# Kernel optimization log

Hardware: AMD Instinct MI355X
Metric: run time of the kernel (lower is better)

The kernel has to match this reference:

```python
import jax, jax.numpy as jnp
import numpy as np

EPS = 1e-6


def _att_vector(x, W, b, sharp2, th2, is_last):
    """AttentionVector on a 2D payoff slice.
    x: (N, a, m). W: (1, 2), b: (1,). Returns (N, a)."""
    # compare_param: pair (x[n,j,k], x[n,i,k]) -> Linear(2,1) -> sigmoid -> mean over k
    # Linear on the concat pair is w00*x[n,j,k] + w01*x[n,i,k] + b, so we fuse it.
    lin = W[0, 0] * x[:, None, :, :] + W[0, 1] * x[:, :, None, :] + b[0]  # (N,a,a,m)
    c = jnp.mean(jax.nn.sigmoid(lin), axis=3)  # (N,a,a)
    # max_normalize over dim 2
    c = c / (jnp.max(c, axis=2, keepdims=True) + EPS)
    # compute_player_mask
    m = jnp.mean(c, axis=2)  # (N,a)
    m = jax.nn.relu(m * sharp2[0] + th2[0])
    m = jax.nn.softmax(m, axis=1)
    if not is_last:
        m = m / (jnp.max(m, axis=1, keepdims=True) + EPS)
    return m


def setup_inputs() -> dict:
    key = jax.random.key(0)
    ks = jax.random.split(key, 16)
    N, a1, a2, f = 128, 64, 64, 2
    inp = {
        "x": jax.random.normal(ks[0], (N, f, a1, a2), dtype=jnp.float32),
        "fc_W": jax.random.normal(ks[1], (2, 2), dtype=jnp.float32) * 0.5,
        "fc_b": jax.random.normal(ks[2], (2,), dtype=jnp.float32) * 0.1,
        "p1_W": jax.random.normal(ks[3], (1, 2), dtype=jnp.float32) * 0.5,
        "p1_b": jax.random.normal(ks[4], (1,), dtype=jnp.float32) * 0.1,
        "p1_sharp": jnp.ones((1,), dtype=jnp.float32),
        "p1_th": jnp.zeros((1,), dtype=jnp.float32),
        "p2_W": jax.random.normal(ks[5], (1, 2), dtype=jnp.float32) * 0.5,
        "p2_b": jax.random.normal(ks[6], (1,), dtype=jnp.float32) * 0.1,
        "p2_sharp": jnp.ones((1,), dtype=jnp.float32),
        "p2_th": jnp.zeros((1,), dtype=jnp.float32),
        "out_W": jax.random.normal(ks[7], (1, 2), dtype=jnp.float32) * 0.5,
        "out_b": jax.random.normal(ks[8], (1,), dtype=jnp.float32) * 0.1,
        "out_sharp": jnp.ones((1,), dtype=jnp.float32),
        "out_th": jnp.zeros((1,), dtype=jnp.float32),
    }
    return inp


def reference(x, fc_W, fc_b, p1_W, p1_b, p1_sharp, p1_th,
              p2_W, p2_b, p2_sharp, p2_th,
              out_W, out_b, out_sharp, out_th):
    # x: (N, f=2, a1, a2) -> (N, a1, a2, f)
    h = jnp.transpose(x, (0, 2, 3, 1))
    # is_fc_first: Linear(2, 2) + ReLU on last dim
    h = jax.nn.relu(h @ fc_W.T + fc_b)  # (N,a1,a2,2)
    # one AttentionModule (module_layers=1, not simult)
    vec1 = _att_vector(h[..., 0], p1_W, p1_b, p1_sharp, p1_th, is_last=False)  # (N,a1)
    h = h * vec1[:, :, None, None]
    pl2 = jnp.transpose(h[..., 1], (0, 2, 1))  # (N,a2,a1)
    vec2 = _att_vector(pl2, p2_W, p2_b, p2_sharp, p2_th, is_last=False)  # (N,a2)
    h = h * vec2[:, None, :, None]
    # with_last: final AttentionVector (is_last=True) on player-1 channel
    out = _att_vector(h[..., 0], out_W, out_b, out_sharp, out_th, is_last=True)  # (N,a1)
    return out
```

## Files before the change

### kernel.cpp

```cpp
#include <hip/hip_runtime.h>


constexpr int A   = 64;
constexpr int PAD = 68;
constexpr float L2E  = 1.4426950408889634f;
constexpr float EPSF = 1e-6f;

__device__ __forceinline__ float bcast(float v, int srcLane) {
    return __int_as_float(__builtin_amdgcn_readlane(__float_as_int(v), srcLane));
}
__device__ __forceinline__ float rcpf(float v) { return __builtin_amdgcn_rcpf(v); }
__device__ __forceinline__ float ex2(float v)  { return __builtin_amdgcn_exp2f(v); }

template <int CTRL>
__device__ __forceinline__ float upd_dpp(float src) {
    return __int_as_float(__builtin_amdgcn_update_dpp(
        0, __float_as_int(src), CTRL, 0xF, 0xF, true));
}
__device__ __forceinline__ float wave_sum64(float x) {
    x += upd_dpp<0x111>(x);
    x += upd_dpp<0x112>(x);
    x += upd_dpp<0x114>(x);
    x += upd_dpp<0x118>(x);
    x += upd_dpp<0x142>(x);
    x += upd_dpp<0x143>(x);
    return bcast(x, 63);
}
__device__ __forceinline__ float wave_max64(float x) {
    x = fmaxf(x, upd_dpp<0x111>(x));
    x = fmaxf(x, upd_dpp<0x112>(x));
    x = fmaxf(x, upd_dpp<0x114>(x));
    x = fmaxf(x, upd_dpp<0x118>(x));
    x = fmaxf(x, upd_dpp<0x142>(x));
    x = fmaxf(x, upd_dpp<0x143>(x));
    return bcast(x, 63);
}

__device__ __forceinline__ void att2q(const float* __restrict__ prow,
                                      const float* __restrict__ qL,
                                      int row0, int lane,
                                      float* __restrict__ mbuf,
                                      float* __restrict__ mg)
{
    const float qreg0 = qL[row0 * PAD + lane];
    const float qreg1 = qL[(row0 + 1) * PAD + lane];
    float acc0 = 0.f, acc1 = 0.f;
#pragma unroll 1
    for (int c = 0; c < 4; ++c) {
        float pk[16];
        *(float4*)(&pk[0])  = *(const float4*)(prow + c * 16 + 0);
        *(float4*)(&pk[4])  = *(const float4*)(prow + c * 16 + 4);
        *(float4*)(&pk[8])  = *(const float4*)(prow + c * 16 + 8);
        *(float4*)(&pk[12]) = *(const float4*)(prow + c * 16 + 12);
#pragma unroll
        for (int t = 0; t < 8; ++t) {
            const int k0 = c * 16 + 2 * t, k1 = k0 + 1;
            {
                float u0 = fmaf(pk[2 * t],     bcast(qreg0, k0), 1.0f);
                float u1 = fmaf(pk[2 * t + 1], bcast(qreg0, k1), 1.0f);
                acc0 = fmaf(u0 + u1, rcpf(u0 * u1), acc0);
            }
            {
                float u0 = fmaf(pk[2 * t],     bcast(qreg1, k0), 1.0f);
                float u1 = fmaf(pk[2 * t + 1], bcast(qreg1, k1), 1.0f);
                acc1 = fmaf(u0 + u1, rcpf(u0 * u1), acc1);
            }
        }
    }
    const float s0 = wave_sum64(acc0), m0 = wave_max64(acc0);
    const float s1 = wave_sum64(acc1), m1 = wave_max64(acc1);
    if (lane == 0) {
        float v0 = (s0 * (1.0f / 4096.0f)) / (m0 * (1.0f / 64.0f) + EPSF);
        float v1 = (s1 * (1.0f / 4096.0f)) / (m1 * (1.0f / 64.0f) + EPSF);
        mbuf[row0]     = v0;
        mbuf[row0 + 1] = v1;
        __hip_atomic_store(mg + row0,     v0 + 2.0f, __ATOMIC_RELAXED, __HIP_MEMORY_SCOPE_AGENT);
        __hip_atomic_store(mg + row0 + 1, v1 + 2.0f, __ATOMIC_RELAXED, __HIP_MEMORY_SCOPE_AGENT);
    }
}

__device__ __forceinline__ float softmax64(float m, float sharp, float th, bool last)
{
    float v = fmaxf(0.f, m * sharp + th);
    float mx = wave_max64(v);
    float e = __expf(v - mx);
    float s = wave_sum64(e);
    float r = e / s;
    if (!last) {
        float rm = wave_max64(r);
        r = r / (rm + EPSF);
    }
    return r;
}

__device__ __forceinline__ float exch_soft(const float* __restrict__ mbuf,
                                           const float* __restrict__ mg,
                                           int half, int lane,
                                           float sharp, float th, bool last)
{
    float mv;
    if ((lane >> 5) == half) {
        mv = mbuf[lane];
    } else {
        const float* p = mg + lane;
        for (;;) {
            float f = __hip_atomic_load(p, __ATOMIC_RELAXED, __HIP_MEMORY_SCOPE_AGENT);
            unsigned u = __float_as_uint(f);
            if ((u >> 23) == 0x80u) { mv = f - 2.0f; break; }
            __builtin_amdgcn_s_sleep(1);
        }
    }
    return softmax64(mv, sharp, th, last);
}

__global__ __launch_bounds__(1024, 2)
void attn_half(const float* __restrict__ x,
               const float* __restrict__ fcW, const float* __restrict__ fcb,
               const float* __restrict__ p1W, const float* __restrict__ p1b,
               const float* __restrict__ p1s, const float* __restrict__ p1t,
               const float* __restrict__ p2W, const float* __restrict__ p2b,
               const float* __restrict__ p2s, const float* __restrict__ p2t,
               const float* __restrict__ oW,  const float* __restrict__ ob,
               const float* __restrict__ os,  const float* __restrict__ ot,
               float* __restrict__ mglob,
               float* __restrict__ out)
{
    __shared__ __align__(16) float pL[A * PAD];
    __shared__ __align__(16) float qL[A * PAD];
    __shared__ float mbuf[A];
    __shared__ float v1buf[A], v2buf[A];

    const int tid = threadIdx.x, lane = tid & 63, wv = tid >> 6;
    const int n = blockIdx.x >> 1, half = blockIdx.x & 1;
    const int row0 = half * 32 + wv * 2;
    const int i = tid >> 4, j = (tid & 15) * 4;
    float* mg = mglob + (size_t)n * 3 * A;

    const float4* x0v = (const float4*)(x + (size_t)n * 2 * A * A);
    const float4* x1v = x0v + (A * A / 4);
    const float4 a = x0v[tid];
    const float4 c = x1v[tid];
    const float w00 = fcW[0], w01 = fcW[1], w10 = fcW[2], w11 = fcW[3];
    const float b0 = fcb[0], b1 = fcb[1];
    const float h0v[4] = { fmaxf(0.f, w00 * a.x + w01 * c.x + b0),
                           fmaxf(0.f, w00 * a.y + w01 * c.y + b0),
                           fmaxf(0.f, w00 * a.z + w01 * c.z + b0),
                           fmaxf(0.f, w00 * a.w + w01 * c.w + b0) };
    const float h1v[4] = { fmaxf(0.f, w10 * a.x + w11 * c.x + b1),
                           fmaxf(0.f, w10 * a.y + w11 * c.y + b1),
                           fmaxf(0.f, w10 * a.z + w11 * c.z + b1),
                           fmaxf(0.f, w10 * a.w + w11 * c.w + b1) };

    {
        const float W0 = p1W[0], W1 = p1W[1], bb = p1b[0];
        float4 pv, qv;
        pv.x = ex2(-L2E * (W0 * h0v[0] + bb)); qv.x = ex2(-L2E * (W1 * h0v[0]));
        pv.y = ex2(-L2E * (W0 * h0v[1] + bb)); qv.y = ex2(-L2E * (W1 * h0v[1]));
        pv.z = ex2(-L2E * (W0 * h0v[2] + bb)); qv.z = ex2(-L2E * (W1 * h0v[2]));
        pv.w = ex2(-L2E * (W0 * h0v[3] + bb)); qv.w = ex2(-L2E * (W1 * h0v[3]));
        *(float4*)&pL[i * PAD + j] = pv;
        *(float4*)&qL[i * PAD + j] = qv;
    }
    __syncthreads();
    att2q(pL + lane * PAD, qL, row0, lane, mbuf, mg);
    __syncthreads();
    if (wv == 0) v1buf[lane] = exch_soft(mbuf, mg, half, lane, p1s[0], p1t[0], false);
    __syncthreads();

    {
        const float W0 = p2W[0], W1 = p2W[1], bb = p2b[0];
        const float sc = v1buf[i];
#pragma unroll
        for (int t = 0; t < 4; ++t) {
            float hv = h1v[t] * sc;
            pL[(j + t) * PAD + i] = ex2(-L2E * (W0 * hv + bb));
            qL[(j + t) * PAD + i] = ex2(-L2E * (W1 * hv));
        }
    }
    __syncthreads();
    att2q(pL + lane * PAD, qL, row0, lane, mbuf, mg + A);
    __syncthreads();
    if (wv == 0) v2buf[lane] = exch_soft(mbuf, mg + A, half, lane, p2s[0], p2t[0], false);
    __syncthreads();

    {
        const float W0 = oW[0], W1 = oW[1], bb = ob[0];
        const float sc = v1buf[i];
        const float4 v2q = *(const float4*)&v2buf[j];
        float hv0 = h0v[0] * sc * v2q.x, hv1 = h0v[1] * sc * v2q.y;
        float hv2 = h0v[2] * sc * v2q.z, hv3 = h0v[3] * sc * v2q.w;
        float4 pv, qv;
        pv.x = ex2(-L2E * (W0 * hv0 + bb)); qv.x = ex2(-L2E * (W1 * hv0));
        pv.y = ex2(-L2E * (W0 * hv1 + bb)); qv.y = ex2(-L2E * (W1 * hv1));
        pv.z = ex2(-L2E * (W0 * hv2 + bb)); qv.z = ex2(-L2E * (W1 * hv2));
        pv.w = ex2(-L2E * (W0 * hv3 + bb)); qv.w = ex2(-L2E * (W1 * hv3));
        *(float4*)&pL[i * PAD + j] = pv;
        *(float4*)&qL[i * PAD + j] = qv;
    }
    __syncthreads();
    att2q(pL + lane * PAD, qL, row0, lane, mbuf, mg + 2 * A);
    __syncthreads();

    if (wv == 0) {
        float r = exch_soft(mbuf, mg + 2 * A, half, lane, os[0], ot[0], true);
        if ((lane >> 5) == half) out[(size_t)n * A + lane] = r;
    }
}

extern "C" void kernel_launch(void* const* d_in, const int* in_sizes, int n_in,
                              void* d_out, int out_size, void* d_ws, size_t ws_size,
                              hipStream_t stream)
{
    (void)n_in; (void)out_size; (void)ws_size;
    const float* x   = (const float*)d_in[0];
    const float* fcW = (const float*)d_in[1];
    const float* fcb = (const float*)d_in[2];
    const float* p1W = (const float*)d_in[3];
    const float* p1b = (const float*)d_in[4];
    const float* p1s = (const float*)d_in[5];
    const float* p1t = (const float*)d_in[6];
    const float* p2W = (const float*)d_in[7];
    const float* p2b = (const float*)d_in[8];
    const float* p2s = (const float*)d_in[9];
    const float* p2t = (const float*)d_in[10];
    const float* oW  = (const float*)d_in[11];
    const float* ob  = (const float*)d_in[12];
    const float* os  = (const float*)d_in[13];
    const float* ot  = (const float*)d_in[14];
    float* out = (float*)d_out;

    const int N = in_sizes[0] / (2 * A * A);
    float* mglob = (float*)d_ws;

    attn_half<<<2 * N, 1024, 0, stream>>>(x, fcW, fcb,
                                          p1W, p1b, p1s, p1t,
                                          p2W, p2b, p2s, p2t,
                                          oW, ob, os, ot, mglob, out);
}
```

Measured before the change: 102.3 us.

## Split each sample across four 512-thread blocks instead of two 1024-thread blocks

Each sample is now handled by four cooperating blocks of 512 threads. Each block owns 16 rows of the comparison matrix and exchanges its partial means through global memory with the other three. Every thread now loads and transforms 8 elements instead of 4. The goal is more blocks and more occupancy on the GPU with smaller per-block synchronisation. In exchange, every block still recomputes the whole 64x64 exp tables, so that work is duplicated four times, and there is more spin-waiting on cross-block flags.

```diff
diff --git a/kernel.cpp b/kernel.cpp
--- a/kernel.cpp
+++ b/kernel.cpp
@@ -95,11 +95,11 @@
 
 __device__ __forceinline__ float exch_soft(const float* __restrict__ mbuf,
                                            const float* __restrict__ mg,
-                                           int half, int lane,
+                                           int qtr, int lane,
                                            float sharp, float th, bool last)
 {
     float mv;
-    if ((lane >> 5) == half) {
+    if ((lane >> 4) == qtr) {
         mv = mbuf[lane];
     } else {
         const float* p = mg + lane;
@@ -113,17 +113,17 @@
     return softmax64(mv, sharp, th, last);
 }
 
-__global__ __launch_bounds__(1024, 2)
-void attn_half(const float* __restrict__ x,
-               const float* __restrict__ fcW, const float* __restrict__ fcb,
-               const float* __restrict__ p1W, const float* __restrict__ p1b,
-               const float* __restrict__ p1s, const float* __restrict__ p1t,
-               const float* __restrict__ p2W, const float* __restrict__ p2b,
-               const float* __restrict__ p2s, const float* __restrict__ p2t,
-               const float* __restrict__ oW,  const float* __restrict__ ob,
-               const float* __restrict__ os,  const float* __restrict__ ot,
-               float* __restrict__ mglob,
-               float* __restrict__ out)
+__global__ __launch_bounds__(512, 4)
+void attn_qtr(const float* __restrict__ x,
+              const float* __restrict__ fcW, const float* __restrict__ fcb,
+              const float* __restrict__ p1W, const float* __restrict__ p1b,
+              const float* __restrict__ p1s, const float* __restrict__ p1t,
+              const float* __restrict__ p2W, const float* __restrict__ p2b,
+              const float* __restrict__ p2s, const float* __restrict__ p2t,
+              const float* __restrict__ oW,  const float* __restrict__ ob,
+              const float* __restrict__ os,  const float* __restrict__ ot,
+              float* __restrict__ mglob,
+              float* __restrict__ out)
 {
     __shared__ __align__(16) float pL[A * PAD];
     __shared__ __align__(16) float qL[A * PAD];
@@ -131,79 +131,83 @@
     __shared__ float v1buf[A], v2buf[A];
 
     const int tid = threadIdx.x, lane = tid & 63, wv = tid >> 6;
-    const int n = blockIdx.x >> 1, half = blockIdx.x & 1;
-    const int row0 = half * 32 + wv * 2;
-    const int i = tid >> 4, j = (tid & 15) * 4;
+    const int n = blockIdx.x >> 2, qtr = blockIdx.x & 3;
+    const int row0 = qtr * 16 + wv * 2;
+    const int ti = tid >> 3, tj = (tid & 7) * 8;
     float* mg = mglob + (size_t)n * 3 * A;
 
     const float4* x0v = (const float4*)(x + (size_t)n * 2 * A * A);
     const float4* x1v = x0v + (A * A / 4);
-    const float4 a = x0v[tid];
-    const float4 c = x1v[tid];
+    const float4 a0 = x0v[2 * tid], a1 = x0v[2 * tid + 1];
+    const float4 c0 = x1v[2 * tid], c1 = x1v[2 * tid + 1];
     const float w00 = fcW[0], w01 = fcW[1], w10 = fcW[2], w11 = fcW[3];
     const float b0 = fcb[0], b1 = fcb[1];
-    const float h0v[4] = { fmaxf(0.f, w00 * a.x + w01 * c.x + b0),
-                           fmaxf(0.f, w00 * a.y + w01 * c.y + b0),
-                           fmaxf(0.f, w00 * a.z + w01 * c.z + b0),
-                           fmaxf(0.f, w00 * a.w + w01 * c.w + b0) };
-    const float h1v[4] = { fmaxf(0.f, w10 * a.x + w11 * c.x + b1),
-                           fmaxf(0.f, w10 * a.y + w11 * c.y + b1),
-                           fmaxf(0.f, w10 * a.z + w11 * c.z + b1),
-                           fmaxf(0.f, w10 * a.w + w11 * c.w + b1) };
+    const float xs0[8] = { a0.x, a0.y, a0.z, a0.w, a1.x, a1.y, a1.z, a1.w };
+    const float xs1[8] = { c0.x, c0.y, c0.z, c0.w, c1.x, c1.y, c1.z, c1.w };
+    float h0v[8], h1v[8];
+#pragma unroll
+    for (int t = 0; t < 8; ++t) {
+        h0v[t] = fmaxf(0.f, w00 * xs0[t] + w01 * xs1[t] + b0);
+        h1v[t] = fmaxf(0.f, w10 * xs0[t] + w11 * xs1[t] + b1);
+    }
 
     {
         const float W0 = p1W[0], W1 = p1W[1], bb = p1b[0];
-        float4 pv, qv;
-        pv.x = ex2(-L2E * (W0 * h0v[0] + bb)); qv.x = ex2(-L2E * (W1 * h0v[0]));
-        pv.y = ex2(-L2E * (W0 * h0v[1] + bb)); qv.y = ex2(-L2E * (W1 * h0v[1]));
-        pv.z = ex2(-L2E * (W0 * h0v[2] + bb)); qv.z = ex2(-L2E * (W1 * h0v[2]));
-        pv.w = ex2(-L2E * (W0 * h0v[3] + bb)); qv.w = ex2(-L2E * (W1 * h0v[3]));
-        *(float4*)&pL[i * PAD + j] = pv;
-        *(float4*)&qL[i * PAD + j] = qv;
+        float pv[8], qv[8];
+#pragma unroll
+        for (int t = 0; t < 8; ++t) {
+            pv[t] = ex2(-L2E * (W0 * h0v[t] + bb));
+            qv[t] = ex2(-L2E * (W1 * h0v[t]));
+        }
+        *(float4*)&pL[ti * PAD + tj]     = *(float4*)&pv[0];
+        *(float4*)&pL[ti * PAD + tj + 4] = *(float4*)&pv[4];
+        *(float4*)&qL[ti * PAD + tj]     = *(float4*)&qv[0];
+        *(float4*)&qL[ti * PAD + tj + 4] = *(float4*)&qv[4];
     }
     __syncthreads();
     att2q(pL + lane * PAD, qL, row0, lane, mbuf, mg);
     __syncthreads();
-    if (wv == 0) v1buf[lane] = exch_soft(mbuf, mg, half, lane, p1s[0], p1t[0], false);
+    if (wv == 0) v1buf[lane] = exch_soft(mbuf, mg, qtr, lane, p1s[0], p1t[0], false);
     __syncthreads();
 
     {
         const float W0 = p2W[0], W1 = p2W[1], bb = p2b[0];
-        const float sc = v1buf[i];
-#pragma unroll
-        for (int t = 0; t < 4; ++t) {
+        const float sc = v1buf[ti];
+#pragma unroll
+        for (int t = 0; t < 8; ++t) {
             float hv = h1v[t] * sc;
-            pL[(j + t) * PAD + i] = ex2(-L2E * (W0 * hv + bb));
-            qL[(j + t) * PAD + i] = ex2(-L2E * (W1 * hv));
+            pL[(tj + t) * PAD + ti] = ex2(-L2E * (W0 * hv + bb));
+            qL[(tj + t) * PAD + ti] = ex2(-L2E * (W1 * hv));
         }
     }
     __syncthreads();
     att2q(pL + lane * PAD, qL, row0, lane, mbuf, mg + A);
     __syncthreads();
-    if (wv == 0) v2buf[lane] = exch_soft(mbuf, mg + A, half, lane, p2s[0], p2t[0], false);
+    if (wv == 0) v2buf[lane] = exch_soft(mbuf, mg + A, qtr, lane, p2s[0], p2t[0], false);
     __syncthreads();
 
     {
         const float W0 = oW[0], W1 = oW[1], bb = ob[0];
-        const float sc = v1buf[i];
-        const float4 v2q = *(const float4*)&v2buf[j];
-        float hv0 = h0v[0] * sc * v2q.x, hv1 = h0v[1] * sc * v2q.y;
-        float hv2 = h0v[2] * sc * v2q.z, hv3 = h0v[3] * sc * v2q.w;
-        float4 pv, qv;
-        pv.x = ex2(-L2E * (W0 * hv0 + bb)); qv.x = ex2(-L2E * (W1 * hv0));
-        pv.y = ex2(-L2E * (W0 * hv1 + bb)); qv.y = ex2(-L2E * (W1 * hv1));
-        pv.z = ex2(-L2E * (W0 * hv2 + bb)); qv.z = ex2(-L2E * (W1 * hv2));
-        pv.w = ex2(-L2E * (W0 * hv3 + bb)); qv.w = ex2(-L2E * (W1 * hv3));
-        *(float4*)&pL[i * PAD + j] = pv;
-        *(float4*)&qL[i * PAD + j] = qv;
+        const float sc = v1buf[ti];
+        float pv[8], qv[8];
+#pragma unroll
+        for (int t = 0; t < 8; ++t) {
+            float hv = h0v[t] * sc * v2buf[tj + t];
+            pv[t] = ex2(-L2E * (W0 * hv + bb));
+            qv[t] = ex2(-L2E * (W1 * hv));
+        }
+        *(float4*)&pL[ti * PAD + tj]     = *(float4*)&pv[0];
+        *(float4*)&pL[ti * PAD + tj + 4] = *(float4*)&pv[4];
+        *(float4*)&qL[ti * PAD + tj]     = *(float4*)&qv[0];
+        *(float4*)&qL[ti * PAD + tj + 4] = *(float4*)&qv[4];
     }
     __syncthreads();
     att2q(pL + lane * PAD, qL, row0, lane, mbuf, mg + 2 * A);
     __syncthreads();
 
     if (wv == 0) {
-        float r = exch_soft(mbuf, mg + 2 * A, half, lane, os[0], ot[0], true);
-        if ((lane >> 5) == half) out[(size_t)n * A + lane] = r;
+        float r = exch_soft(mbuf, mg + 2 * A, qtr, lane, os[0], ot[0], true);
+        if ((lane >> 4) == qtr) out[(size_t)n * A + lane] = r;
     }
 }
 
@@ -232,8 +236,8 @@
     const int N = in_sizes[0] / (2 * A * A);
     float* mglob = (float*)d_ws;
 
-    attn_half<<<2 * N, 1024, 0, stream>>>(x, fcW, fcb,
-                                          p1W, p1b, p1s, p1t,
-                                          p2W, p2b, p2s, p2t,
-                                          oW, ob, os, ot, mglob, out);
-}
+    attn_qtr<<<4 * N, 512, 0, stream>>>(x, fcW, fcb,
+                                        p1W, p1b, p1s, p1t,
+                                        p2W, p2b, p2s, p2t,
+                                        oW, ob, os, ot, mglob, out);
+}
```

Result: slower. 104.4 us (+2.1%).

## Have every wave poll global mask and compute softmax redundantly, dropping shared buffers and barriers

Applied to the files above, without the earlier changes.

Each wave now polls all 64 mask entries from the global exchange buffer with a wave-wide all-ready check and computes the softmax in registers. This replaces the wave-0-only exchange followed by shared-memory broadcast, which removes two __syncthreads per stage and the LDS buffers. Per-row scale factors are then pulled out of registers with readlane/shuffle. Only block half 0 writes the final output. Launch bounds also change to request 4 blocks per CU. The cost is that every wave spins on global memory and does the softmax redundantly, which adds memory-polling traffic.

```diff
diff --git a/kernel.cpp b/kernel.cpp
--- a/kernel.cpp
+++ b/kernel.cpp
@@ -39,7 +39,6 @@
 __device__ __forceinline__ void att2q(const float* __restrict__ prow,
                                       const float* __restrict__ qL,
                                       int row0, int lane,
-                                      float* __restrict__ mbuf,
                                       float* __restrict__ mg)
 {
     const float qreg0 = qL[row0 * PAD + lane];
@@ -72,10 +71,18 @@
     if (lane == 0) {
         float v0 = (s0 * (1.0f / 4096.0f)) / (m0 * (1.0f / 64.0f) + EPSF);
         float v1 = (s1 * (1.0f / 4096.0f)) / (m1 * (1.0f / 64.0f) + EPSF);
-        mbuf[row0]     = v0;
-        mbuf[row0 + 1] = v1;
         __hip_atomic_store(mg + row0,     v0 + 2.0f, __ATOMIC_RELAXED, __HIP_MEMORY_SCOPE_AGENT);
         __hip_atomic_store(mg + row0 + 1, v1 + 2.0f, __ATOMIC_RELAXED, __HIP_MEMORY_SCOPE_AGENT);
+    }
+}
+
+__device__ __forceinline__ float poll_all(const float* __restrict__ mg, int lane)
+{
+    for (;;) {
+        float f = __hip_atomic_load(mg + lane, __ATOMIC_RELAXED, __HIP_MEMORY_SCOPE_AGENT);
+        unsigned u = __float_as_uint(f);
+        if (__all((u >> 23) == 0x80u)) return f - 2.0f;
+        __builtin_amdgcn_s_sleep(1);
     }
 }
 
@@ -93,27 +100,19 @@
     return r;
 }
 
-__device__ __forceinline__ float exch_soft(const float* __restrict__ mbuf,
-                                           const float* __restrict__ mg,
-                                           int half, int lane,
-                                           float sharp, float th, bool last)
-{
-    float mv;
-    if ((lane >> 5) == half) {
-        mv = mbuf[lane];
-    } else {
-        const float* p = mg + lane;
-        for (;;) {
-            float f = __hip_atomic_load(p, __ATOMIC_RELAXED, __HIP_MEMORY_SCOPE_AGENT);
-            unsigned u = __float_as_uint(f);
-            if ((u >> 23) == 0x80u) { mv = f - 2.0f; break; }
-            __builtin_amdgcn_s_sleep(1);
-        }
-    }
-    return softmax64(mv, sharp, th, last);
-}
-
-__global__ __launch_bounds__(1024, 2)
+__device__ __forceinline__ float gather4(float v, int wv, int lane)
+{
+    float r0 = bcast(v, 4 * wv + 0);
+    float r1 = bcast(v, 4 * wv + 1);
+    float r2 = bcast(v, 4 * wv + 2);
+    float r3 = bcast(v, 4 * wv + 3);
+    int g = (lane >> 4) & 3;
+    float lo = (g & 1) ? r1 : r0;
+    float hi = (g & 1) ? r3 : r2;
+    return (g & 2) ? hi : lo;
+}
+
+__global__ __launch_bounds__(1024, 4)
 void attn_half(const float* __restrict__ x,
                const float* __restrict__ fcW, const float* __restrict__ fcb,
                const float* __restrict__ p1W, const float* __restrict__ p1b,
@@ -127,8 +126,6 @@
 {
     __shared__ __align__(16) float pL[A * PAD];
     __shared__ __align__(16) float qL[A * PAD];
-    __shared__ float mbuf[A];
-    __shared__ float v1buf[A], v2buf[A];
 
     const int tid = threadIdx.x, lane = tid & 63, wv = tid >> 6;
     const int n = blockIdx.x >> 1, half = blockIdx.x & 1;
@@ -162,48 +159,44 @@
         *(float4*)&qL[i * PAD + j] = qv;
     }
     __syncthreads();
-    att2q(pL + lane * PAD, qL, row0, lane, mbuf, mg);
-    __syncthreads();
-    if (wv == 0) v1buf[lane] = exch_soft(mbuf, mg, half, lane, p1s[0], p1t[0], false);
-    __syncthreads();
-
+    att2q(pL + lane * PAD, qL, row0, lane, mg);
+    const float v1reg = softmax64(poll_all(mg, lane), p1s[0], p1t[0], false);
+    __syncthreads();
+
+    const float sc1 = gather4(v1reg, wv, lane);
     {
         const float W0 = p2W[0], W1 = p2W[1], bb = p2b[0];
-        const float sc = v1buf[i];
 #pragma unroll
         for (int t = 0; t < 4; ++t) {
-            float hv = h1v[t] * sc;
+            float hv = h1v[t] * sc1;
             pL[(j + t) * PAD + i] = ex2(-L2E * (W0 * hv + bb));
             qL[(j + t) * PAD + i] = ex2(-L2E * (W1 * hv));
         }
     }
     __syncthreads();
-    att2q(pL + lane * PAD, qL, row0, lane, mbuf, mg + A);
-    __syncthreads();
-    if (wv == 0) v2buf[lane] = exch_soft(mbuf, mg + A, half, lane, p2s[0], p2t[0], false);
+    att2q(pL + lane * PAD, qL, row0, lane, mg + A);
+    const float v2reg = softmax64(poll_all(mg + A, lane), p2s[0], p2t[0], false);
     __syncthreads();
 
     {
         const float W0 = oW[0], W1 = oW[1], bb = ob[0];
-        const float sc = v1buf[i];
-        const float4 v2q = *(const float4*)&v2buf[j];
-        float hv0 = h0v[0] * sc * v2q.x, hv1 = h0v[1] * sc * v2q.y;
-        float hv2 = h0v[2] * sc * v2q.z, hv3 = h0v[3] * sc * v2q.w;
-        float4 pv, qv;
-        pv.x = ex2(-L2E * (W0 * hv0 + bb)); qv.x = ex2(-L2E * (W1 * hv0));
-        pv.y = ex2(-L2E * (W0 * hv1 + bb)); qv.y = ex2(-L2E * (W1 * hv1));
-        pv.z = ex2(-L2E * (W0 * hv2 + bb)); qv.z = ex2(-L2E * (W1 * hv2));
-        pv.w = ex2(-L2E * (W0 * hv3 + bb)); qv.w = ex2(-L2E * (W1 * hv3));
-        *(float4*)&pL[i * PAD + j] = pv;
-        *(float4*)&qL[i * PAD + j] = qv;
-    }
-    __syncthreads();
-    att2q(pL + lane * PAD, qL, row0, lane, mbuf, mg + 2 * A);
-    __syncthreads();
-
-    if (wv == 0) {
-        float r = exch_soft(mbuf, mg + 2 * A, half, lane, os[0], ot[0], true);
-        if ((lane >> 5) == half) out[(size_t)n * A + lane] = r;
+        float pv[4], qv[4];
+#pragma unroll
+        for (int t = 0; t < 4; ++t) {
+            float v2t = __shfl(v2reg, j + t, 64);
+            float hv = h0v[t] * sc1 * v2t;
+            pv[t] = ex2(-L2E * (W0 * hv + bb));
+            qv[t] = ex2(-L2E * (W1 * hv));
+        }
+        *(float4*)&pL[i * PAD + j] = *(float4*)&pv[0];
+        *(float4*)&qL[i * PAD + j] = *(float4*)&qv[0];
+    }
+    __syncthreads();
+    att2q(pL + lane * PAD, qL, row0, lane, mg + 2 * A);
+
+    if (half == 0 && wv == 0) {
+        float r = softmax64(poll_all(mg + 2 * A, lane), os[0], ot[0], true);
+        out[(size_t)n * A + lane] = r;
     }
 }
 
```

Result: slower. 106.3 us (+3.9%).
